# Optimization experiments

Hardware: AMD Instinct MI355X
Metric: run time of the kernel (lower is better)

Reference implementation:

```python
import jax, jax.numpy as jnp
import numpy as np

B, S, D = 8, 2048, 768
N_SPANS = 512
MAX_W = 30  # static max span width (inclusive width in tokens)
H = 100
NEG = -1e30


def setup_inputs() -> dict:
    key = jax.random.key(0)
    k1, k2, k3, k4, k5, k6 = jax.random.split(key, 6)
    seq_tensor = jax.random.normal(k1, (B, S, D), dtype=jnp.float32)
    starts = jax.random.randint(k2, (B, N_SPANS), 0, S - MAX_W)
    widths = jax.random.randint(k3, (B, N_SPANS), 1, MAX_W + 1)  # span length in [1, MAX_W]
    ends_excl = starts + widths  # exclusive end, as module expects
    span_indices = jnp.stack([starts, ends_excl], axis=-1).astype(jnp.int64)
    span_mask = (jax.random.uniform(k4, (B, N_SPANS)) > 0.1).astype(jnp.int32)
    att_w = jax.random.normal(k5, (D, 1), dtype=jnp.float32) / np.sqrt(D)
    att_b = jnp.zeros((1,), dtype=jnp.float32)
    ffnn_w = jax.random.normal(k6, (D, H), dtype=jnp.float32) / np.sqrt(D)
    ffnn_b = jnp.zeros((H,), dtype=jnp.float32)
    return {"seq_tensor": seq_tensor, "span_indices": span_indices, "span_mask": span_mask,
            "att_w": att_w, "att_b": att_b, "ffnn_w": ffnn_w, "ffnn_b": ffnn_b}


def reference(seq_tensor, span_indices, span_mask, att_w, att_b, ffnn_w, ffnn_b):
    # exclusive end -> inclusive end (span_end_is_exclusive=True)
    starts = span_indices[..., 0]
    ends = span_indices[..., 1] - 1
    widths = ends - starts  # inclusive width - 1, in [0, MAX_W-1]

    offsets = jnp.arange(MAX_W)  # [W]
    raw_idx = starts[..., None] + offsets  # [B, N, W]
    width_mask = offsets <= widths[..., None]  # [B, N, W]
    idx = jnp.where(width_mask, raw_idx, 0)

    # global attention logits over the sequence: [B, S]
    att_logits = (jnp.einsum('bsd,do->bso', seq_tensor, att_w) + att_b)[..., 0]

    # gather span token embeddings and logits: [B, N, W, D], [B, N, W]
    span_emb = jax.vmap(lambda seq, i: seq[i])(seq_tensor, idx)
    span_logits = jax.vmap(lambda lg, i: lg[i])(att_logits, idx)

    # masked softmax over span width
    span_logits = jnp.where(width_mask, span_logits, NEG)
    attn = jax.nn.softmax(span_logits, axis=-1)  # [B, N, W]

    attended = jnp.einsum('bnw,bnwd->bnd', attn, span_emb)  # [B, N, D]
    attended = attended * span_mask.astype(attended.dtype)[..., None]

    # FeedForward: 1 layer Linear + tanh (dropout=0)
    out = jnp.tanh(jnp.einsum('bnd,dh->bnh', attended, ffnn_w) + ffnn_b)
    return out
```

## Files before the change

### kernel.cpp

```cpp
#include <hip/hip_runtime.h>
#include <cstdint>
#include <cstddef>

#define NB 8
#define NS 2048
#define ND 768
#define NSP 512
#define MAXW 30
#define NH 100
#define LDP 104
#define NKS 24
#define NCF 8
#define BM 32
#define NIT 12

typedef __attribute__((ext_vector_type(8))) _Float16 half8;
typedef __attribute__((ext_vector_type(2))) __fp16 fp16x2;
typedef __attribute__((ext_vector_type(4))) float floatx4;

union U4H8 { uint4 v; half8 h8; unsigned u[4]; unsigned short us[8]; };
union H2U  { fp16x2 h; unsigned u; };

__device__ inline unsigned short f2h(float f) {
    _Float16 h = (_Float16)f;
    union { _Float16 hh; unsigned short us; } c; c.hh = h;
    return c.us;
}

__global__ __launch_bounds__(64) void pack_b_kernel(
    const float* __restrict__ ffnn_w, const float* __restrict__ att_w,
    uint4* __restrict__ Bfrag)
{
    const int ks = blockIdx.x >> 3, cf = blockIdx.x & 7;
    const int lane = threadIdx.x;
    const int q = lane >> 4, r = lane & 15;
    const int n = cf * 16 + r;
    U4H8 p;
#pragma unroll
    for (int j = 0; j < 8; j++) {
        int k = ks * 32 + q * 8 + j;
        float v = (n < NH) ? ffnn_w[(size_t)k * NH + n]
                           : (n == NH ? att_w[k] : 0.f);
        p.us[j] = f2h(v);
    }
    Bfrag[(size_t)(ks * NCF + cf) * 64 + lane] = p.v;
}

__global__ __launch_bounds__(256, 4) void proj_kernel(
    const float* __restrict__ seq, const uint4* __restrict__ Bfrag,
    float* __restrict__ P, float* __restrict__ Lg)
{
    __shared__ unsigned Ah[2][BM][36];
    const int t = threadIdx.x;
    const int wave = t >> 6, lane = t & 63;
    const int q = lane >> 4, r = lane & 15;
    const int cf0 = wave * 2;
    const int row0 = blockIdx.x * BM;

    floatx4 acc[2][2] = {{{0.f,0.f,0.f,0.f},{0.f,0.f,0.f,0.f}},
                         {{0.f,0.f,0.f,0.f},{0.f,0.f,0.f,0.f}}};

    const int sr = t >> 3, sc = t & 7;
    const float4* gA = (const float4*)(seq + (size_t)(row0 + sr) * ND);
    float4 sv0 = gA[sc], sv1 = gA[sc + 8];

    const uint4* bp = Bfrag + (size_t)cf0 * 64 + lane;
    uint4 Bc0 = bp[0], Bc1 = bp[64], Bc2 = bp[512], Bc3 = bp[512 + 64];

    for (int i = 0; i < NIT; ++i) {
        H2U a01, a23, b01, b23;
        a01.h = __builtin_amdgcn_cvt_pkrtz(sv0.x, sv0.y);
        a23.h = __builtin_amdgcn_cvt_pkrtz(sv0.z, sv0.w);
        b01.h = __builtin_amdgcn_cvt_pkrtz(sv1.x, sv1.y);
        b23.h = __builtin_amdgcn_cvt_pkrtz(sv1.z, sv1.w);
        { uint2 u; u.x = a01.u; u.y = a23.u; *(uint2*)&Ah[i & 1][sr][sc * 2] = u; }
        { uint2 u; u.x = b01.u; u.y = b23.u; *(uint2*)&Ah[i & 1][sr][sc * 2 + 16] = u; }
        __syncthreads();

        const int ni = (i + 1 < NIT) ? i + 1 : i;
        sv0 = gA[ni * 16 + sc];
        sv1 = gA[ni * 16 + sc + 8];
        const size_t nb = (size_t)ni * 1024;
        uint4 Bn0 = bp[nb], Bn1 = bp[nb + 64], Bn2 = bp[nb + 512], Bn3 = bp[nb + 512 + 64];

#pragma unroll
        for (int ksl = 0; ksl < 2; ++ksl) {
            U4H8 b0, b1;
            b0.v = ksl ? Bc2 : Bc0;
            b1.v = ksl ? Bc3 : Bc1;
#pragma unroll
            for (int rt = 0; rt < 2; ++rt) {
                U4H8 a;
                a.v = *(const uint4*)&Ah[i & 1][rt * 16 + r][ksl * 16 + q * 4];
                acc[rt][0] = __builtin_amdgcn_mfma_f32_16x16x32_f16(a.h8, b0.h8, acc[rt][0], 0, 0, 0);
                acc[rt][1] = __builtin_amdgcn_mfma_f32_16x16x32_f16(a.h8, b1.h8, acc[rt][1], 0, 0, 0);
            }
        }
        Bc0 = Bn0; Bc1 = Bn1; Bc2 = Bn2; Bc3 = Bn3;
    }

#pragma unroll
    for (int rt = 0; rt < 2; ++rt) {
#pragma unroll
        for (int c = 0; c < 2; ++c) {
            const int col = (cf0 + c) * 16 + r;
            const int rowb = row0 + rt * 16 + q * 4;
            if (col < NH) {
#pragma unroll
                for (int reg = 0; reg < 4; ++reg)
                    P[(size_t)(rowb + reg) * LDP + col] = acc[rt][c][reg];
            } else if (col == NH) {
#pragma unroll
                for (int reg = 0; reg < 4; ++reg)
                    Lg[rowb + reg] = acc[rt][c][reg];
            }
        }
    }
}

__global__ __launch_bounds__(256, 4) void span_kernel(
    const int* __restrict__ span_idx, const int* __restrict__ span_mask,
    const float* __restrict__ P, const float* __restrict__ Lg,
    const float* __restrict__ ffnn_b, float* __restrict__ out)
{
    const int wave = threadIdx.x >> 6;
    const int lane = threadIdx.x & 63;
    const int half = lane >> 5, l32 = lane & 31;
    const int gs = blockIdx.x * 4 + wave;
    const int b = gs / NSP;
    const int st = span_idx[2 * gs];
    int w = span_idx[2 * gs + 1] - st;
    w = max(1, min(w, MAXW));

    float lg = (l32 < w) ? Lg[b * NS + st + l32] : -1e30f;
    float mx = lg;
#pragma unroll
    for (int off = 16; off > 0; off >>= 1) mx = fmaxf(mx, __shfl_xor(mx, off, 32));
    float e = (l32 < w) ? __expf(lg - mx) : 0.f;
    float sum = e;
#pragma unroll
    for (int off = 16; off > 0; off >>= 1) sum += __shfl_xor(sum, off, 32);
    float attn = e / sum;

    const int cl = min(l32, 24);
    const float4* Pb4 = (const float4*)(P + ((size_t)b * NS + st) * LDP) + cl;
    float4 acc = {0.f, 0.f, 0.f, 0.f};
#pragma unroll
    for (int j = 0; j < MAXW / 2; ++j) {
        const int row = 2 * j + half;
        float a = __shfl(attn, row, 32);
        if (row < w) {
            float4 v = Pb4[row * (LDP / 4)];
            acc.x += a * v.x; acc.y += a * v.y; acc.z += a * v.z; acc.w += a * v.w;
        }
    }
    acc.x += __shfl_xor(acc.x, 32, 64);
    acc.y += __shfl_xor(acc.y, 32, 64);
    acc.z += __shfl_xor(acc.z, 32, 64);
    acc.w += __shfl_xor(acc.w, 32, 64);

    if (half == 0 && l32 < 25) {
        float m = (float)span_mask[gs];
        float4 bias = ((const float4*)ffnn_b)[cl];
        float4 o;
        o.x = tanhf(m * acc.x + bias.x);
        o.y = tanhf(m * acc.y + bias.y);
        o.z = tanhf(m * acc.z + bias.z);
        o.w = tanhf(m * acc.w + bias.w);
        *(float4*)(out + (size_t)gs * NH + 4 * l32) = o;
    }
}

extern "C" void kernel_launch(void* const* d_in, const int* in_sizes, int n_in,
                              void* d_out, int out_size, void* d_ws, size_t ws_size,
                              hipStream_t stream) {
    const float* seq      = (const float*)d_in[0];
    const int*   span_idx = (const int*)d_in[1];
    const int*   span_msk = (const int*)d_in[2];
    const float* att_w    = (const float*)d_in[3];
    const float* ffnn_w   = (const float*)d_in[5];
    const float* ffnn_b   = (const float*)d_in[6];
    float* out = (float*)d_out;

    char* ws = (char*)d_ws;
    size_t off = 0;
    float* P     = (float*)(ws + off); off += (size_t)NB * NS * LDP * 4;
    uint4* Bfrag = (uint4*)(ws + off); off += (size_t)NKS * NCF * 64 * 16;
    float* Lg    = (float*)(ws + off);

    pack_b_kernel<<<NKS * NCF, 64, 0, stream>>>(ffnn_w, att_w, Bfrag);
    proj_kernel<<<(NB * NS) / BM, 256, 0, stream>>>(seq, Bfrag, P, Lg);
    span_kernel<<<(NB * NSP) / 4, 256, 0, stream>>>(span_idx, span_msk, P, Lg, ffnn_b, out);
}
```

Before: 111.1 us.

## Fuse pack, projection and span kernels into one cooperative kernel

Merges the three kernels into one cooperative launch of 512 blocks, separated by two grid-wide barriers. Weight packing runs in the first 48 blocks, then the projection GEMM, then the span softmax/weighted sum with each block handling 8 spans. The aim is to remove the overhead of separate kernel launches and the gaps between them. The cost is two grid syncs, and all 512 blocks must be co-resident, which depends on the launch-bounds occupancy hint of 2 blocks per CU.

```diff
diff --git a/kernel.cpp b/kernel.cpp
--- a/kernel.cpp
+++ b/kernel.cpp
@@ -1,6 +1,9 @@
 #include <hip/hip_runtime.h>
+#include <hip/hip_cooperative_groups.h>
 #include <cstdint>
 #include <cstddef>
+
+namespace cg = cooperative_groups;
 
 #define NB 8
 #define NS 2048
@@ -27,147 +30,153 @@
     return c.us;
 }
 
-__global__ __launch_bounds__(64) void pack_b_kernel(
-    const float* __restrict__ ffnn_w, const float* __restrict__ att_w,
-    uint4* __restrict__ Bfrag)
-{
-    const int ks = blockIdx.x >> 3, cf = blockIdx.x & 7;
-    const int lane = threadIdx.x;
-    const int q = lane >> 4, r = lane & 15;
-    const int n = cf * 16 + r;
-    U4H8 p;
-#pragma unroll
-    for (int j = 0; j < 8; j++) {
-        int k = ks * 32 + q * 8 + j;
-        float v = (n < NH) ? ffnn_w[(size_t)k * NH + n]
-                           : (n == NH ? att_w[k] : 0.f);
-        p.us[j] = f2h(v);
-    }
-    Bfrag[(size_t)(ks * NCF + cf) * 64 + lane] = p.v;
-}
-
-__global__ __launch_bounds__(256, 4) void proj_kernel(
-    const float* __restrict__ seq, const uint4* __restrict__ Bfrag,
-    float* __restrict__ P, float* __restrict__ Lg)
+__global__ __launch_bounds__(256, 2) void fused_kernel(
+    const float* __restrict__ seq,
+    const int* __restrict__ span_idx, const int* __restrict__ span_mask,
+    const float* __restrict__ att_w, const float* __restrict__ ffnn_w,
+    const float* __restrict__ ffnn_b,
+    uint4* __restrict__ Bfrag, float* __restrict__ P, float* __restrict__ Lg,
+    float* __restrict__ out)
 {
     __shared__ unsigned Ah[2][BM][36];
     const int t = threadIdx.x;
     const int wave = t >> 6, lane = t & 63;
-    const int q = lane >> 4, r = lane & 15;
-    const int cf0 = wave * 2;
-    const int row0 = blockIdx.x * BM;
-
-    floatx4 acc[2][2] = {{{0.f,0.f,0.f,0.f},{0.f,0.f,0.f,0.f}},
-                         {{0.f,0.f,0.f,0.f},{0.f,0.f,0.f,0.f}}};
-
-    const int sr = t >> 3, sc = t & 7;
-    const float4* gA = (const float4*)(seq + (size_t)(row0 + sr) * ND);
-    float4 sv0 = gA[sc], sv1 = gA[sc + 8];
-
-    const uint4* bp = Bfrag + (size_t)cf0 * 64 + lane;
-    uint4 Bc0 = bp[0], Bc1 = bp[64], Bc2 = bp[512], Bc3 = bp[512 + 64];
-
-    for (int i = 0; i < NIT; ++i) {
-        H2U a01, a23, b01, b23;
-        a01.h = __builtin_amdgcn_cvt_pkrtz(sv0.x, sv0.y);
-        a23.h = __builtin_amdgcn_cvt_pkrtz(sv0.z, sv0.w);
-        b01.h = __builtin_amdgcn_cvt_pkrtz(sv1.x, sv1.y);
-        b23.h = __builtin_amdgcn_cvt_pkrtz(sv1.z, sv1.w);
-        { uint2 u; u.x = a01.u; u.y = a23.u; *(uint2*)&Ah[i & 1][sr][sc * 2] = u; }
-        { uint2 u; u.x = b01.u; u.y = b23.u; *(uint2*)&Ah[i & 1][sr][sc * 2 + 16] = u; }
-        __syncthreads();
-
-        const int ni = (i + 1 < NIT) ? i + 1 : i;
-        sv0 = gA[ni * 16 + sc];
-        sv1 = gA[ni * 16 + sc + 8];
-        const size_t nb = (size_t)ni * 1024;
-        uint4 Bn0 = bp[nb], Bn1 = bp[nb + 64], Bn2 = bp[nb + 512], Bn3 = bp[nb + 512 + 64];
-
-#pragma unroll
-        for (int ksl = 0; ksl < 2; ++ksl) {
-            U4H8 b0, b1;
-            b0.v = ksl ? Bc2 : Bc0;
-            b1.v = ksl ? Bc3 : Bc1;
-#pragma unroll
-            for (int rt = 0; rt < 2; ++rt) {
-                U4H8 a;
-                a.v = *(const uint4*)&Ah[i & 1][rt * 16 + r][ksl * 16 + q * 4];
-                acc[rt][0] = __builtin_amdgcn_mfma_f32_16x16x32_f16(a.h8, b0.h8, acc[rt][0], 0, 0, 0);
-                acc[rt][1] = __builtin_amdgcn_mfma_f32_16x16x32_f16(a.h8, b1.h8, acc[rt][1], 0, 0, 0);
-            }
-        }
-        Bc0 = Bn0; Bc1 = Bn1; Bc2 = Bn2; Bc3 = Bn3;
+    cg::grid_group grid = cg::this_grid();
+
+    if (blockIdx.x < 48) {
+        const int gw = blockIdx.x * 4 + wave;
+        const int ks = gw >> 3, cf = gw & 7;
+        const int q = lane >> 4, r = lane & 15;
+        const int n = cf * 16 + r;
+        U4H8 p;
+#pragma unroll
+        for (int j = 0; j < 8; j++) {
+            int k = ks * 32 + q * 8 + j;
+            float v = (n < NH) ? ffnn_w[(size_t)k * NH + n]
+                               : (n == NH ? att_w[k] : 0.f);
+            p.us[j] = f2h(v);
+        }
+        Bfrag[(size_t)(ks * NCF + cf) * 64 + lane] = p.v;
     }
-
-#pragma unroll
-    for (int rt = 0; rt < 2; ++rt) {
-#pragma unroll
-        for (int c = 0; c < 2; ++c) {
-            const int col = (cf0 + c) * 16 + r;
-            const int rowb = row0 + rt * 16 + q * 4;
-            if (col < NH) {
-#pragma unroll
-                for (int reg = 0; reg < 4; ++reg)
-                    P[(size_t)(rowb + reg) * LDP + col] = acc[rt][c][reg];
-            } else if (col == NH) {
-#pragma unroll
-                for (int reg = 0; reg < 4; ++reg)
-                    Lg[rowb + reg] = acc[rt][c][reg];
+    __threadfence();
+    grid.sync();
+
+    {
+        const int q = lane >> 4, r = lane & 15;
+        const int cf0 = wave * 2;
+        const int row0 = blockIdx.x * BM;
+
+        floatx4 acc[2][2] = {{{0.f,0.f,0.f,0.f},{0.f,0.f,0.f,0.f}},
+                             {{0.f,0.f,0.f,0.f},{0.f,0.f,0.f,0.f}}};
+
+        const int sr = t >> 3, sc = t & 7;
+        const float4* gA = (const float4*)(seq + (size_t)(row0 + sr) * ND);
+        float4 sv0 = gA[sc], sv1 = gA[sc + 8];
+
+        const uint4* bp = Bfrag + (size_t)cf0 * 64 + lane;
+        uint4 Bc0 = bp[0], Bc1 = bp[64], Bc2 = bp[512], Bc3 = bp[512 + 64];
+
+        for (int i = 0; i < NIT; ++i) {
+            H2U a01, a23, b01, b23;
+            a01.h = __builtin_amdgcn_cvt_pkrtz(sv0.x, sv0.y);
+            a23.h = __builtin_amdgcn_cvt_pkrtz(sv0.z, sv0.w);
+            b01.h = __builtin_amdgcn_cvt_pkrtz(sv1.x, sv1.y);
+            b23.h = __builtin_amdgcn_cvt_pkrtz(sv1.z, sv1.w);
+            { uint2 u; u.x = a01.u; u.y = a23.u; *(uint2*)&Ah[i & 1][sr][sc * 2] = u; }
+            { uint2 u; u.x = b01.u; u.y = b23.u; *(uint2*)&Ah[i & 1][sr][sc * 2 + 16] = u; }
+            __syncthreads();
+
+            const int ni = (i + 1 < NIT) ? i + 1 : i;
+            sv0 = gA[ni * 16 + sc];
+            sv1 = gA[ni * 16 + sc + 8];
+            const size_t nb = (size_t)ni * 1024;
+            uint4 Bn0 = bp[nb], Bn1 = bp[nb + 64], Bn2 = bp[nb + 512], Bn3 = bp[nb + 512 + 64];
+
+#pragma unroll
+            for (int ksl = 0; ksl < 2; ++ksl) {
+                U4H8 b0, b1;
+                b0.v = ksl ? Bc2 : Bc0;
+                b1.v = ksl ? Bc3 : Bc1;
+#pragma unroll
+                for (int rt = 0; rt < 2; ++rt) {
+                    U4H8 a;
+                    a.v = *(const uint4*)&Ah[i & 1][rt * 16 + r][ksl * 16 + q * 4];
+                    acc[rt][0] = __builtin_amdgcn_mfma_f32_16x16x32_f16(a.h8, b0.h8, acc[rt][0], 0, 0, 0);
+                    acc[rt][1] = __builtin_amdgcn_mfma_f32_16x16x32_f16(a.h8, b1.h8, acc[rt][1], 0, 0, 0);
+                }
+            }
+            Bc0 = Bn0; Bc1 = Bn1; Bc2 = Bn2; Bc3 = Bn3;
+        }
+
+#pragma unroll
+        for (int rt = 0; rt < 2; ++rt) {
+#pragma unroll
+            for (int c = 0; c < 2; ++c) {
+                const int col = (cf0 + c) * 16 + r;
+                const int rowb = row0 + rt * 16 + q * 4;
+                if (col < NH) {
+#pragma unroll
+                    for (int reg = 0; reg < 4; ++reg)
+                        P[(size_t)(rowb + reg) * LDP + col] = acc[rt][c][reg];
+                } else if (col == NH) {
+#pragma unroll
+                    for (int reg = 0; reg < 4; ++reg)
+                        Lg[rowb + reg] = acc[rt][c][reg];
+                }
             }
         }
     }
-}
-
-__global__ __launch_bounds__(256, 4) void span_kernel(
-    const int* __restrict__ span_idx, const int* __restrict__ span_mask,
-    const float* __restrict__ P, const float* __restrict__ Lg,
-    const float* __restrict__ ffnn_b, float* __restrict__ out)
-{
-    const int wave = threadIdx.x >> 6;
-    const int lane = threadIdx.x & 63;
-    const int half = lane >> 5, l32 = lane & 31;
-    const int gs = blockIdx.x * 4 + wave;
-    const int b = gs / NSP;
-    const int st = span_idx[2 * gs];
-    int w = span_idx[2 * gs + 1] - st;
-    w = max(1, min(w, MAXW));
-
-    float lg = (l32 < w) ? Lg[b * NS + st + l32] : -1e30f;
-    float mx = lg;
-#pragma unroll
-    for (int off = 16; off > 0; off >>= 1) mx = fmaxf(mx, __shfl_xor(mx, off, 32));
-    float e = (l32 < w) ? __expf(lg - mx) : 0.f;
-    float sum = e;
-#pragma unroll
-    for (int off = 16; off > 0; off >>= 1) sum += __shfl_xor(sum, off, 32);
-    float attn = e / sum;
-
-    const int cl = min(l32, 24);
-    const float4* Pb4 = (const float4*)(P + ((size_t)b * NS + st) * LDP) + cl;
-    float4 acc = {0.f, 0.f, 0.f, 0.f};
-#pragma unroll
-    for (int j = 0; j < MAXW / 2; ++j) {
-        const int row = 2 * j + half;
-        float a = __shfl(attn, row, 32);
-        if (row < w) {
-            float4 v = Pb4[row * (LDP / 4)];
-            acc.x += a * v.x; acc.y += a * v.y; acc.z += a * v.z; acc.w += a * v.w;
-        }
-    }
-    acc.x += __shfl_xor(acc.x, 32, 64);
-    acc.y += __shfl_xor(acc.y, 32, 64);
-    acc.z += __shfl_xor(acc.z, 32, 64);
-    acc.w += __shfl_xor(acc.w, 32, 64);
-
-    if (half == 0 && l32 < 25) {
-        float m = (float)span_mask[gs];
-        float4 bias = ((const float4*)ffnn_b)[cl];
-        float4 o;
-        o.x = tanhf(m * acc.x + bias.x);
-        o.y = tanhf(m * acc.y + bias.y);
-        o.z = tanhf(m * acc.z + bias.z);
-        o.w = tanhf(m * acc.w + bias.w);
-        *(float4*)(out + (size_t)gs * NH + 4 * l32) = o;
+    __threadfence();
+    grid.sync();
+
+    {
+        const int half = lane >> 5, l32 = lane & 31;
+#pragma unroll
+        for (int j2 = 0; j2 < 2; ++j2) {
+            const int gs = blockIdx.x * 8 + wave * 2 + j2;
+            const int b = gs / NSP;
+            const int st = span_idx[2 * gs];
+            int w = span_idx[2 * gs + 1] - st;
+            w = max(1, min(w, MAXW));
+
+            float lg = (l32 < w) ? Lg[b * NS + st + l32] : -1e30f;
+            float mx = lg;
+#pragma unroll
+            for (int off = 16; off > 0; off >>= 1) mx = fmaxf(mx, __shfl_xor(mx, off, 32));
+            float e = (l32 < w) ? __expf(lg - mx) : 0.f;
+            float sum = e;
+#pragma unroll
+            for (int off = 16; off > 0; off >>= 1) sum += __shfl_xor(sum, off, 32);
+            float attn = e / sum;
+
+            const int cl = min(l32, 24);
+            const float4* Pb4 = (const float4*)(P + ((size_t)b * NS + st) * LDP) + cl;
+            float4 acc = {0.f, 0.f, 0.f, 0.f};
+#pragma unroll
+            for (int j = 0; j < MAXW / 2; ++j) {
+                const int row = 2 * j + half;
+                float a = __shfl(attn, row, 32);
+                if (row < w) {
+                    float4 v = Pb4[row * (LDP / 4)];
+                    acc.x += a * v.x; acc.y += a * v.y; acc.z += a * v.z; acc.w += a * v.w;
+                }
+            }
+            acc.x += __shfl_xor(acc.x, 32, 64);
+            acc.y += __shfl_xor(acc.y, 32, 64);
+            acc.z += __shfl_xor(acc.z, 32, 64);
+            acc.w += __shfl_xor(acc.w, 32, 64);
+
+            if (half == 0 && l32 < 25) {
+                float m = (float)span_mask[gs];
+                float4 bias = ((const float4*)ffnn_b)[cl];
+                float4 o;
+                o.x = tanhf(m * acc.x + bias.x);
+                o.y = tanhf(m * acc.y + bias.y);
+                o.z = tanhf(m * acc.z + bias.z);
+                o.w = tanhf(m * acc.w + bias.w);
+                *(float4*)(out + (size_t)gs * NH + 4 * l32) = o;
+            }
+        }
     }
 }
 
@@ -188,7 +197,9 @@
     uint4* Bfrag = (uint4*)(ws + off); off += (size_t)NKS * NCF * 64 * 16;
     float* Lg    = (float*)(ws + off);
 
-    pack_b_kernel<<<NKS * NCF, 64, 0, stream>>>(ffnn_w, att_w, Bfrag);
-    proj_kernel<<<(NB * NS) / BM, 256, 0, stream>>>(seq, Bfrag, P, Lg);
-    span_kernel<<<(NB * NSP) / 4, 256, 0, stream>>>(span_idx, span_msk, P, Lg, ffnn_b, out);
+    void* args[] = { (void*)&seq, (void*)&span_idx, (void*)&span_msk, (void*)&att_w,
+                     (void*)&ffnn_w, (void*)&ffnn_b, (void*)&Bfrag, (void*)&P,
+                     (void*)&Lg, (void*)&out };
+    hipLaunchCooperativeKernel((const void*)fused_kernel, dim3((NB * NS) / BM),
+                               dim3(256), args, 0, stream);
 }
```

After: 307.7 us. 177% more time.
